# Kernel tuning notes

Hardware: AMD Instinct MI355X
Metric: run time of the kernel (lower is better)

## Reference

```python
import jax, jax.numpy as jnp
import numpy as np

N_NODES = 50000
N_EDGES = 640000
IN_DIM = 128
OUT_DIM = 128
EDGE_DIM = 16
N_HEADS = 4
HEAD_DIM = OUT_DIM // N_HEADS  # 32
LN_EPS = 1e-5


def setup_inputs() -> dict:
    key = jax.random.key(0)
    ks = jax.random.split(key, 6)
    h = jax.random.normal(ks[0], (N_NODES, IN_DIM), dtype=jnp.float32)
    edge_index = jax.random.randint(ks[1], (2, N_EDGES), 0, N_NODES, dtype=jnp.int64)
    edge_feat = jax.random.normal(ks[2], (N_EDGES, EDGE_DIM), dtype=jnp.float32)
    # parameters (xavier-ish scaling)
    W = jax.random.normal(ks[3], (OUT_DIM, IN_DIM), dtype=jnp.float32) * (1.0 / np.sqrt(IN_DIM))
    W_e = jax.random.normal(ks[4], (N_HEADS, EDGE_DIM), dtype=jnp.float32) * (1.0 / np.sqrt(EDGE_DIM))
    a = jax.random.normal(ks[5], (N_HEADS, 2 * HEAD_DIM), dtype=jnp.float32) * (1.0 / np.sqrt(2 * HEAD_DIM))
    ln_scale = jnp.ones((OUT_DIM,), dtype=jnp.float32)
    ln_bias = jnp.zeros((OUT_DIM,), dtype=jnp.float32)
    return {"h": h, "edge_index": edge_index, "edge_feat": edge_feat,
            "W": W, "W_e": W_e, "a": a, "ln_scale": ln_scale, "ln_bias": ln_bias}


def _layer_norm(x, scale, bias):
    mu = jnp.mean(x, axis=-1, keepdims=True)
    var = jnp.mean(jnp.square(x - mu), axis=-1, keepdims=True)
    return (x - mu) * jax.lax.rsqrt(var + LN_EPS) * scale + bias


def reference(h, edge_index, edge_feat, W, W_e, a, ln_scale, ln_bias):
    N = h.shape[0]
    H, D = N_HEADS, HEAD_DIM
    src, dst = edge_index[0], edge_index[1]

    Wh = (h @ W.T).reshape(N, H, D)                       # [N,H,D]
    Wh_src = Wh[src]                                       # [E,H,D] gather
    Wh_dst = Wh[dst]                                       # [E,H,D] gather
    # e_ij = leaky_relu(a . [Wh_src || Wh_dst]) + W_e . edge_feat
    attn = (jnp.concatenate([Wh_src, Wh_dst], axis=-1) * a[None]).sum(-1)  # [E,H]
    attn = jax.nn.leaky_relu(attn, negative_slope=0.2)
    attn = attn + edge_feat @ W_e.T                        # [E,H]

    # scatter-softmax over incoming edges per destination node
    max_v = jax.ops.segment_max(attn, dst, num_segments=N)   # [N,H]
    max_v = jnp.maximum(max_v, -1e9)                         # match torch init
    exp_v = jnp.exp(attn - max_v[dst])                       # [E,H]
    denom = jax.ops.segment_sum(exp_v, dst, num_segments=N)  # [N,H]
    alpha = exp_v / (denom[dst] + 1e-9)                      # [E,H]

    # per-head scatter-add aggregation: h_i' = sum_j alpha_ij * Wh_j
    agg = jax.ops.segment_sum(alpha[..., None] * Wh_src, dst, num_segments=N)  # [N,H,D]
    out = agg.reshape(N, H * D)
    return _layer_norm(jax.nn.gelu(out, approximate=False), ln_scale, ln_bias)
```

## Files before the change

kernel.cpp:

```cpp
#include <hip/hip_runtime.h>
#include <math.h>

#define N_NODES 50000
#define N_EDGES 640000
#define DIM 128
#define EDGE_DIM 16
#define N_HEADS 4
#define HEAD_DIM 32
#define CAPB 48

typedef __attribute__((ext_vector_type(8))) short bf16x8;
typedef __attribute__((ext_vector_type(4))) float floatx4;

__device__ __forceinline__ unsigned short f2bf(float f) {
    unsigned int x = __float_as_uint(f);
    unsigned int r = (x + 0x7FFFu + ((x >> 16) & 1u)) >> 16;
    return (unsigned short)r;
}
__device__ __forceinline__ float bfu2f_lo(unsigned int u) {
    return __uint_as_float(u << 16);
}
__device__ __forceinline__ float bfu2f_hi(unsigned int u) {
    return __uint_as_float(u & 0xFFFF0000u);
}

__global__ __launch_bounds__(256) void k_prep(
    const float* __restrict__ W, const float* __restrict__ a,
    unsigned short* __restrict__ Wbf, unsigned short* __restrict__ Pbf,
    int* __restrict__ counts)
{
    int b = blockIdx.x, t = threadIdx.x;
    if (b < 64) {
        int i = b * 256 + t;
        Wbf[i] = f2bf(W[i]);
    } else if (b < 260) {
        int i = (b - 64) * 256 + t;
        if (i < N_NODES) counts[i] = 0;
    } else {
        int idx = (b - 260) * 256 + t;
        int j = idx >> 7, c = idx & 127;
        int hh = j & 3, off = (j >> 2) * 32;
        float dot = 0.f;
#pragma unroll
        for (int d = 0; d < 32; ++d)
            dot += W[(size_t)(hh * 32 + d) * DIM + c] * a[hh * 64 + off + d];
        Pbf[j * DIM + c] = f2bf(dot);
        Pbf[(j + 8) * DIM + c] = 0;
    }
}

__global__ __launch_bounds__(256) void k_gemm(
    const float* __restrict__ h,
    const unsigned short* __restrict__ Wbf,
    const unsigned short* __restrict__ Pbf,
    unsigned short* __restrict__ Whbf,
    float* __restrict__ sc)
{
    int wave = threadIdx.x >> 6;
    int lane = threadIdx.x & 63;
    int nb = blockIdx.x * 64 + wave * 16;
    int m = lane & 15;
    int q = lane >> 4;

    int node = nb + m;
    bool nvalid = node < N_NODES;

    bf16x8 hfrag[4];
#pragma unroll
    for (int kt = 0; kt < 4; ++kt) {
        bf16x8 f;
        if (nvalid) {
            const float* p = h + (size_t)node * DIM + kt * 32 + q * 8;
            float4 x0 = *(const float4*)(p);
            float4 x1 = *(const float4*)(p + 4);
            f[0] = (short)f2bf(x0.x); f[1] = (short)f2bf(x0.y);
            f[2] = (short)f2bf(x0.z); f[3] = (short)f2bf(x0.w);
            f[4] = (short)f2bf(x1.x); f[5] = (short)f2bf(x1.y);
            f[6] = (short)f2bf(x1.z); f[7] = (short)f2bf(x1.w);
        } else {
#pragma unroll
            for (int j = 0; j < 8; ++j) f[j] = 0;
        }
        hfrag[kt] = f;
    }

    floatx4 accS = {0.f, 0.f, 0.f, 0.f};
#pragma unroll
    for (int kt = 0; kt < 4; ++kt) {
        bf16x8 pfrag = *(const bf16x8*)(Pbf + (size_t)m * DIM + kt * 32 + q * 8);
        accS = __builtin_amdgcn_mfma_f32_16x16x32_bf16(pfrag, hfrag[kt], accS, 0, 0, 0);
    }
    if (q < 2 && nvalid) {
        *(float4*)(sc + (size_t)node * 8 + q * 4) =
            make_float4(accS[0], accS[1], accS[2], accS[3]);
    }

#pragma unroll
    for (int dt = 0; dt < 8; ++dt) {
        floatx4 acc = {0.f, 0.f, 0.f, 0.f};
#pragma unroll
        for (int kt = 0; kt < 4; ++kt) {
            bf16x8 wfrag = *(const bf16x8*)(Wbf + (size_t)(dt * 16 + m) * DIM + kt * 32 + q * 8);
            acc = __builtin_amdgcn_mfma_f32_16x16x32_bf16(wfrag, hfrag[kt], acc, 0, 0, 0);
        }
        if (nvalid) {
            unsigned int lo = ((unsigned int)f2bf(acc[1]) << 16) | f2bf(acc[0]);
            unsigned int hi = ((unsigned int)f2bf(acc[3]) << 16) | f2bf(acc[2]);
            uint2 pk; pk.x = lo; pk.y = hi;
            *(uint2*)(Whbf + (size_t)node * DIM + dt * 16 + q * 4) = pk;
        }
    }
}

__global__ __launch_bounds__(256) void k_scatter(
    const int* __restrict__ ei,
    const float* __restrict__ ef,
    const float* __restrict__ We,
    const float* __restrict__ sc,
    int* __restrict__ counts,
    uint4* __restrict__ brec)
{
    __shared__ float ef_s[256 * 17];
    int t = threadIdx.x;
    int e0 = blockIdx.x * 256;

    const float4* g = (const float4*)(ef + (size_t)e0 * 16);
#pragma unroll
    for (int i = 0; i < 4; ++i) {
        int gidx = i * 256 + t;
        float4 v = g[gidx];
        float* d = ef_s + (gidx >> 2) * 17 + (gidx & 3) * 4;
        d[0] = v.x; d[1] = v.y; d[2] = v.z; d[3] = v.w;
    }
    __syncthreads();

    int e = e0 + t;
    int src = ei[e], dst = ei[N_EDGES + e];
    float4 ss = *(const float4*)(sc + (size_t)src * 8);
    float4 sd = *(const float4*)(sc + (size_t)dst * 8 + 4);
    float lg[4] = {ss.x + sd.x, ss.y + sd.y, ss.z + sd.z, ss.w + sd.w};

    const float* fr = ef_s + t * 17;
#pragma unroll
    for (int hh = 0; hh < 4; ++hh) {
        const float4* wep = (const float4*)(We + hh * 16);
        float4 w0 = wep[0], w1 = wep[1], w2 = wep[2], w3 = wep[3];
        float ed = fr[0]  * w0.x + fr[1]  * w0.y + fr[2]  * w0.z + fr[3]  * w0.w
                 + fr[4]  * w1.x + fr[5]  * w1.y + fr[6]  * w1.z + fr[7]  * w1.w
                 + fr[8]  * w2.x + fr[9]  * w2.y + fr[10] * w2.z + fr[11] * w2.w
                 + fr[12] * w3.x + fr[13] * w3.y + fr[14] * w3.z + fr[15] * w3.w;
        float s = lg[hh];
        s = s > 0.f ? s : 0.2f * s;
        lg[hh] = __expf(s + ed);
    }
    int slot = atomicAdd(counts + dst, 1);
    if (slot < CAPB) {
        uint4 rec;
        rec.x = (unsigned int)src;
        rec.y = ((unsigned int)f2bf(lg[1]) << 16) | f2bf(lg[0]);
        rec.z = ((unsigned int)f2bf(lg[3]) << 16) | f2bf(lg[2]);
        rec.w = 0;
        brec[(size_t)dst * CAPB + slot] = rec;
    }
}

__global__ __launch_bounds__(256) void k_node(
    const int* __restrict__ counts,
    const uint4* __restrict__ brec,
    const unsigned short* __restrict__ Whbf,
    const float* __restrict__ ln_scale, const float* __restrict__ ln_bias,
    float* __restrict__ out)
{
    __shared__ __align__(16) float p_s[4][CAPB * 4];
    __shared__ int s_s[4][CAPB];
    int w = threadIdx.x >> 6, l = threadIdx.x & 63;
    int n = blockIdx.x * 4 + w;
    int deg = counts[n];
    deg = deg < CAPB ? deg : CAPB;
    size_t base = (size_t)n * CAPB;

    if (l < CAPB) {
        uint4 rec = make_uint4(0u, 0u, 0u, 0u);
        if (l < deg) rec = brec[base + l];
        float4 pv;
        pv.x = bfu2f_lo(rec.y); pv.y = bfu2f_hi(rec.y);
        pv.z = bfu2f_lo(rec.z); pv.w = bfu2f_hi(rec.z);
        *(float4*)&p_s[w][l * 4] = pv;
        s_s[w][l] = (int)rec.x;
    }
    __syncthreads();

    int hb = l >> 4;
    float den = 0.f, a0 = 0.f, a1 = 0.f;
    int nch = (deg + 7) >> 3;
    for (int c = 0; c < nch; ++c) {
        int e0 = c * 8;
        float pv[8];
        unsigned int uu[8];
#pragma unroll
        for (int j = 0; j < 8; ++j) {
            int e = e0 + j;
            int src = s_s[w][e];
            pv[j] = p_s[w][e * 4 + hb];
            uu[j] = *(const unsigned int*)(Whbf + (size_t)src * DIM + 2 * l);
        }
#pragma unroll
        for (int j = 0; j < 8; ++j) {
            den += pv[j];
            a0 += pv[j] * bfu2f_lo(uu[j]);
            a1 += pv[j] * bfu2f_hi(uu[j]);
        }
    }
    float dd = den + 1e-9f;
    float x0 = a0 / dd, x1 = a1 / dd;
    float g0 = 0.5f * x0 * (1.f + erff(x0 * 0.70710678118654752f));
    float g1 = 0.5f * x1 * (1.f + erff(x1 * 0.70710678118654752f));
    float s = g0 + g1, ss = g0 * g0 + g1 * g1;
#pragma unroll
    for (int off = 1; off < 64; off <<= 1) {
        s += __shfl_xor(s, off, 64);
        ss += __shfl_xor(ss, off, 64);
    }
    float mu = s * (1.f / 128.f);
    float var = ss * (1.f / 128.f) - mu * mu;
    float rstd = rsqrtf(var + 1e-5f);
    float2 sca = *(const float2*)(ln_scale + 2 * l);
    float2 bi = *(const float2*)(ln_bias + 2 * l);
    float2 o;
    o.x = (g0 - mu) * rstd * sca.x + bi.x;
    o.y = (g1 - mu) * rstd * sca.y + bi.y;
    *(float2*)(out + (size_t)n * DIM + 2 * l) = o;
}

extern "C" void kernel_launch(void* const* d_in, const int* in_sizes, int n_in,
                              void* d_out, int out_size, void* d_ws, size_t ws_size,
                              hipStream_t stream) {
    const float* h   = (const float*)d_in[0];
    const int*   ei  = (const int*)d_in[1];
    const float* ef  = (const float*)d_in[2];
    const float* W   = (const float*)d_in[3];
    const float* We  = (const float*)d_in[4];
    const float* a   = (const float*)d_in[5];
    const float* lsc = (const float*)d_in[6];
    const float* lbi = (const float*)d_in[7];

    char* ws = (char*)d_ws;
    size_t off = 0;
    unsigned short* Wbf  = (unsigned short*)(ws + off); off += (size_t)DIM * DIM * 2;
    unsigned short* Pbf  = (unsigned short*)(ws + off); off += (size_t)16 * DIM * 2;
    unsigned short* Whbf = (unsigned short*)(ws + off); off += (size_t)N_NODES * DIM * 2;
    float* sc    = (float*)(ws + off); off += (size_t)N_NODES * 8 * 4;
    int*   counts= (int*)(ws + off);   off += (size_t)N_NODES * 4;
    uint4* brec  = (uint4*)(ws + off); off += (size_t)N_NODES * CAPB * 16;

    k_prep<<<264, 256, 0, stream>>>(W, a, Wbf, Pbf, counts);
    k_gemm<<<(N_NODES + 63) / 64, 256, 0, stream>>>(h, Wbf, Pbf, Whbf, sc);
    k_scatter<<<N_EDGES / 256, 256, 0, stream>>>(ei, ef, We, sc, counts, brec);
    k_node<<<N_NODES / 4, 256, 0, stream>>>(counts, brec, Whbf, lsc, lbi,
                                            (float*)d_out);
}
```

Before: 203.3 us.

## Fuse prep into GEMM via LDS weights and split node aggregation across two waves

```diff
diff --git a/kernel.cpp b/kernel.cpp
--- a/kernel.cpp
+++ b/kernel.cpp
@@ -14,8 +14,10 @@
 
 __device__ __forceinline__ unsigned short f2bf(float f) {
     unsigned int x = __float_as_uint(f);
-    unsigned int r = (x + 0x7FFFu + ((x >> 16) & 1u)) >> 16;
-    return (unsigned short)r;
+    return (unsigned short)((x + 0x7FFFu + ((x >> 16) & 1u)) >> 16);
+}
+__device__ __forceinline__ float bf2f(unsigned short u) {
+    return __uint_as_float(((unsigned int)u) << 16);
 }
 __device__ __forceinline__ float bfu2f_lo(unsigned int u) {
     return __uint_as_float(u << 16);
@@ -24,44 +26,70 @@
     return __uint_as_float(u & 0xFFFF0000u);
 }
 
-__global__ __launch_bounds__(256) void k_prep(
-    const float* __restrict__ W, const float* __restrict__ a,
-    unsigned short* __restrict__ Wbf, unsigned short* __restrict__ Pbf,
+__global__ __launch_bounds__(256) void k_gemm(
+    const float* __restrict__ h,
+    const float* __restrict__ W,
+    const float* __restrict__ a,
+    unsigned short* __restrict__ Whbf,
+    float* __restrict__ sc,
     int* __restrict__ counts)
 {
-    int b = blockIdx.x, t = threadIdx.x;
-    if (b < 64) {
-        int i = b * 256 + t;
-        Wbf[i] = f2bf(W[i]);
-    } else if (b < 260) {
-        int i = (b - 64) * 256 + t;
-        if (i < N_NODES) counts[i] = 0;
-    } else {
-        int idx = (b - 260) * 256 + t;
-        int j = idx >> 7, c = idx & 127;
+    __shared__ unsigned short w_lds[16 * 128 * 8];
+    __shared__ unsigned short p_lds[16 * 16 * 8];
+    int t = threadIdx.x;
+
+    if (t < 64) {
+        int ci = blockIdx.x * 64 + t;
+        if (ci < N_NODES) counts[ci] = 0;
+    }
+
+    {
+        int r = t >> 1, halfc = t & 1;
+        const float* wr = W + (size_t)r * DIM + halfc * 64;
+#pragma unroll
+        for (int j = 0; j < 8; ++j) {
+            float4 x0 = *(const float4*)(wr + j * 8);
+            float4 x1 = *(const float4*)(wr + j * 8 + 4);
+            bf16x8 f;
+            f[0] = (short)f2bf(x0.x); f[1] = (short)f2bf(x0.y);
+            f[2] = (short)f2bf(x0.z); f[3] = (short)f2bf(x0.w);
+            f[4] = (short)f2bf(x1.x); f[5] = (short)f2bf(x1.y);
+            f[6] = (short)f2bf(x1.z); f[7] = (short)f2bf(x1.w);
+            int ch = halfc * 8 + j;
+            *(bf16x8*)&w_lds[(ch * 128 + r) * 8] = f;
+        }
+    }
+    {
+        unsigned int* p32 = (unsigned int*)p_lds;
+        int ch = t >> 4, sub = t & 15;
+        p32[ch * 64 + 32 + sub] = 0;
+        p32[ch * 64 + 48 + sub] = 0;
+    }
+    __syncthreads();
+
+    if (t < 128) {
+        int j = t & 7, cg = t >> 3;
         int hh = j & 3, off = (j >> 2) * 32;
-        float dot = 0.f;
-#pragma unroll
-        for (int d = 0; d < 32; ++d)
-            dot += W[(size_t)(hh * 32 + d) * DIM + c] * a[hh * 64 + off + d];
-        Pbf[j * DIM + c] = f2bf(dot);
-        Pbf[(j + 8) * DIM + c] = 0;
-    }
-}
-
-__global__ __launch_bounds__(256) void k_gemm(
-    const float* __restrict__ h,
-    const unsigned short* __restrict__ Wbf,
-    const unsigned short* __restrict__ Pbf,
-    unsigned short* __restrict__ Whbf,
-    float* __restrict__ sc)
-{
-    int wave = threadIdx.x >> 6;
-    int lane = threadIdx.x & 63;
+        int rot = t & 7;
+        float dot[8] = {0.f, 0.f, 0.f, 0.f, 0.f, 0.f, 0.f, 0.f};
+        for (int dd = 0; dd < 32; ++dd) {
+            int d = (dd + rot) & 31;
+            bf16x8 wv = *(const bf16x8*)&w_lds[(cg * 128 + hh * 32 + d) * 8];
+            float av = a[hh * 64 + off + d];
+#pragma unroll
+            for (int k = 0; k < 8; ++k)
+                dot[k] += bf2f((unsigned short)wv[k]) * av;
+        }
+        bf16x8 pf;
+#pragma unroll
+        for (int k = 0; k < 8; ++k) pf[k] = (short)f2bf(dot[k]);
+        *(bf16x8*)&p_lds[(cg * 16 + j) * 8] = pf;
+    }
+    __syncthreads();
+
+    int wave = t >> 6, lane = t & 63;
     int nb = blockIdx.x * 64 + wave * 16;
-    int m = lane & 15;
-    int q = lane >> 4;
-
+    int m = lane & 15, q = lane >> 4;
     int node = nb + m;
     bool nvalid = node < N_NODES;
 
@@ -87,7 +115,7 @@
     floatx4 accS = {0.f, 0.f, 0.f, 0.f};
 #pragma unroll
     for (int kt = 0; kt < 4; ++kt) {
-        bf16x8 pfrag = *(const bf16x8*)(Pbf + (size_t)m * DIM + kt * 32 + q * 8);
+        bf16x8 pfrag = *(const bf16x8*)&p_lds[((kt * 4 + q) * 16 + m) * 8];
         accS = __builtin_amdgcn_mfma_f32_16x16x32_bf16(pfrag, hfrag[kt], accS, 0, 0, 0);
     }
     if (q < 2 && nvalid) {
@@ -100,7 +128,7 @@
         floatx4 acc = {0.f, 0.f, 0.f, 0.f};
 #pragma unroll
         for (int kt = 0; kt < 4; ++kt) {
-            bf16x8 wfrag = *(const bf16x8*)(Wbf + (size_t)(dt * 16 + m) * DIM + kt * 32 + q * 8);
+            bf16x8 wfrag = *(const bf16x8*)&w_lds[((kt * 4 + q) * 128 + dt * 16 + m) * 8];
             acc = __builtin_amdgcn_mfma_f32_16x16x32_bf16(wfrag, hfrag[kt], acc, 0, 0, 0);
         }
         if (nvalid) {
@@ -171,37 +199,40 @@
     const float* __restrict__ ln_scale, const float* __restrict__ ln_bias,
     float* __restrict__ out)
 {
-    __shared__ __align__(16) float p_s[4][CAPB * 4];
-    __shared__ int s_s[4][CAPB];
+    __shared__ __align__(16) float p_s[2][CAPB * 4];
+    __shared__ int s_s[2][CAPB];
+    __shared__ float comb[2][64][3];
     int w = threadIdx.x >> 6, l = threadIdx.x & 63;
-    int n = blockIdx.x * 4 + w;
+    int nw = w >> 1, half = w & 1;
+    int n = blockIdx.x * 2 + nw;
     int deg = counts[n];
     deg = deg < CAPB ? deg : CAPB;
     size_t base = (size_t)n * CAPB;
 
-    if (l < CAPB) {
+    if (l < 24) {
+        int slot = half * 24 + l;
         uint4 rec = make_uint4(0u, 0u, 0u, 0u);
-        if (l < deg) rec = brec[base + l];
+        if (slot < deg) rec = brec[base + slot];
         float4 pv;
         pv.x = bfu2f_lo(rec.y); pv.y = bfu2f_hi(rec.y);
         pv.z = bfu2f_lo(rec.z); pv.w = bfu2f_hi(rec.z);
-        *(float4*)&p_s[w][l * 4] = pv;
-        s_s[w][l] = (int)rec.x;
+        *(float4*)&p_s[nw][slot * 4] = pv;
+        s_s[nw][slot] = (int)rec.x;
     }
     __syncthreads();
 
     int hb = l >> 4;
     float den = 0.f, a0 = 0.f, a1 = 0.f;
     int nch = (deg + 7) >> 3;
-    for (int c = 0; c < nch; ++c) {
+    for (int c = half; c < nch; c += 2) {
         int e0 = c * 8;
         float pv[8];
         unsigned int uu[8];
 #pragma unroll
         for (int j = 0; j < 8; ++j) {
             int e = e0 + j;
-            int src = s_s[w][e];
-            pv[j] = p_s[w][e * 4 + hb];
+            int src = s_s[nw][e];
+            pv[j] = p_s[nw][e * 4 + hb];
             uu[j] = *(const unsigned int*)(Whbf + (size_t)src * DIM + 2 * l);
         }
 #pragma unroll
@@ -211,6 +242,18 @@
             a1 += pv[j] * bfu2f_hi(uu[j]);
         }
     }
+    if (half == 1) {
+        comb[nw][l][0] = den;
+        comb[nw][l][1] = a0;
+        comb[nw][l][2] = a1;
+    }
+    __syncthreads();
+    if (half == 1) return;
+
+    den += comb[nw][l][0];
+    a0  += comb[nw][l][1];
+    a1  += comb[nw][l][2];
+
     float dd = den + 1e-9f;
     float x0 = a0 / dd, x1 = a1 / dd;
     float g0 = 0.5f * x0 * (1.f + erff(x0 * 0.70710678118654752f));
@@ -246,16 +289,13 @@
 
     char* ws = (char*)d_ws;
     size_t off = 0;
-    unsigned short* Wbf  = (unsigned short*)(ws + off); off += (size_t)DIM * DIM * 2;
-    unsigned short* Pbf  = (unsigned short*)(ws + off); off += (size_t)16 * DIM * 2;
     unsigned short* Whbf = (unsigned short*)(ws + off); off += (size_t)N_NODES * DIM * 2;
     float* sc    = (float*)(ws + off); off += (size_t)N_NODES * 8 * 4;
     int*   counts= (int*)(ws + off);   off += (size_t)N_NODES * 4;
     uint4* brec  = (uint4*)(ws + off); off += (size_t)N_NODES * CAPB * 16;
 
-    k_prep<<<264, 256, 0, stream>>>(W, a, Wbf, Pbf, counts);
-    k_gemm<<<(N_NODES + 63) / 64, 256, 0, stream>>>(h, Wbf, Pbf, Whbf, sc);
+    k_gemm<<<(N_NODES + 63) / 64, 256, 0, stream>>>(h, W, a, Whbf, sc, counts);
     k_scatter<<<N_EDGES / 256, 256, 0, stream>>>(ei, ef, We, sc, counts, brec);
-    k_node<<<N_NODES / 4, 256, 0, stream>>>(counts, brec, Whbf, lsc, lbi,
+    k_node<<<N_NODES / 2, 256, 0, stream>>>(counts, brec, Whbf, lsc, lbi,
                                             (float*)d_out);
 }
```

New measurement: 205.0 us. Within noise of the previous version (+0.8%).
